# Optimization experiments

Measured on AMD Instinct MI355X. Metric: run time of the kernel, lower is better.

Reference implementation:

```python
import jax, jax.numpy as jnp
import numpy as np

EPS_D = 1e-8   # clamp_min on knn distances
EPS_BN = 1e-5  # BatchNorm eps
K = 3


def _cdist(a, b):
    # a: (B,M,3), b: (B,N,3) -> (B,M,N) euclidean distances
    a2 = jnp.sum(a * a, axis=-1)[:, :, None]
    b2 = jnp.sum(b * b, axis=-1)[:, None, :]
    ab = jnp.einsum('bmd,bnd->bmn', a, b)
    return jnp.sqrt(jnp.maximum(a2 + b2 - 2.0 * ab, 0.0))


def _bn_relu(x, gamma, beta):
    # x: (B,C,N); BatchNorm1d training-mode math (biased batch stats) + ReLU
    mean = jnp.mean(x, axis=(0, 2), keepdims=True)
    var = jnp.mean((x - mean) ** 2, axis=(0, 2), keepdims=True)
    xn = (x - mean) * jax.lax.rsqrt(var + EPS_BN)
    return jax.nn.relu(xn * gamma[None, :, None] + beta[None, :, None])


def setup_inputs() -> dict:
    key = jax.random.key(0)
    ks = jax.random.split(key, 6)
    B, N1, N2, C1, C2 = 8, 8192, 2048, 128, 256
    xyz1 = jax.random.normal(ks[0], (B, N1, 3), dtype=jnp.float32)
    xyz2 = jax.random.normal(ks[1], (B, N2, 3), dtype=jnp.float32)
    feats1 = jax.random.normal(ks[2], (B, C1, N1), dtype=jnp.float32)
    feats2 = jax.random.normal(ks[3], (B, C2, N2), dtype=jnp.float32)
    in_ch = C2 + C1  # 384
    W1 = jax.random.normal(ks[4], (256, in_ch), dtype=jnp.float32) * 0.05
    b1 = jnp.zeros((256,), jnp.float32)
    g1 = jnp.ones((256,), jnp.float32)
    be1 = jnp.zeros((256,), jnp.float32)
    W2 = jax.random.normal(ks[5], (128, 256), dtype=jnp.float32) * 0.05
    b2 = jnp.zeros((128,), jnp.float32)
    g2 = jnp.ones((128,), jnp.float32)
    be2 = jnp.zeros((128,), jnp.float32)
    return {"xyz1": xyz1, "xyz2": xyz2, "feats1": feats1, "feats2": feats2,
            "W1": W1, "b1": b1, "g1": g1, "be1": be1,
            "W2": W2, "b2": b2, "g2": g2, "be2": be2}


def reference(xyz1, xyz2, feats1, feats2, W1, b1, g1, be1, W2, b2, g2, be2):
    # --- KNN interpolation ---
    d = _cdist(xyz1, xyz2)                       # (B,N1,N2)
    _, idx = jax.lax.top_k(-d, K)                # smallest-K indices (B,N1,K)
    knn_d = jnp.take_along_axis(d, idx, axis=2)  # (B,N1,K)
    w = 1.0 / jnp.maximum(knn_d, EPS_D)
    w = w / jnp.sum(w, axis=-1, keepdims=True)
    f2p = jnp.swapaxes(feats2, 1, 2)             # (B,N2,C2)
    neigh = jax.vmap(lambda f, i: f[i])(f2p, idx)  # (B,N1,K,C2)
    out = jnp.einsum('bmk,bmkc->bmc', w, neigh)  # (B,N1,C2)
    out = jnp.swapaxes(out, 1, 2)                # (B,C2,N1)
    out = jnp.concatenate([out, feats1], axis=1) # (B,C2+C1,N1)
    # --- Conv1d(1)-BN-ReLU MLP ---
    h = jnp.einsum('oc,bcn->bon', W1, out) + b1[None, :, None]
    h = _bn_relu(h, g1, be1)
    h = jnp.einsum('oc,bcn->bon', W2, h) + b2[None, :, None]
    h = _bn_relu(h, g2, be2)
    return h
```

## Files before the change

kernel.cpp:

```cpp
#include <hip/hip_runtime.h>

typedef __attribute__((ext_vector_type(8))) short short8;
typedef __attribute__((ext_vector_type(4))) float f32x4;

#define GLDS(gp, lp) __builtin_amdgcn_global_load_lds( \
    (const __attribute__((address_space(1))) void*)(gp), \
    (__attribute__((address_space(3))) void*)(lp), 16, 0, 0)

__device__ __forceinline__ unsigned short f2bf(float f){
    unsigned u = __float_as_uint(f);
    unsigned r = (u + 0x7fffu + ((u >> 16) & 1u)) >> 16;
    return (unsigned short)r;
}
__device__ __forceinline__ float bf2f(unsigned short s){
    return __uint_as_float(((unsigned)s) << 16);
}

__global__ __launch_bounds__(256) void cast_w_kernel(const float* __restrict__ W1, const float* __restrict__ W2,
                                                     unsigned short* __restrict__ W1c, unsigned short* __restrict__ W2c){
    int i = blockIdx.x * 256 + threadIdx.x;
    if (i < 98304) W1c[i] = f2bf(W1[i]);
    if (i < 32768) W2c[i] = f2bf(W2[i]);
}

__global__ void zero_stats_kernel(float* __restrict__ s){
    int i = blockIdx.x * 256 + threadIdx.x;
    if (i < 768) s[i] = 0.f;
}

__global__ __launch_bounds__(256) void knn_kernel(const float* __restrict__ xyz1, const float* __restrict__ xyz2,
                                                  int* __restrict__ oi, float* __restrict__ ow){
    __shared__ float sx[2048], sy[2048], sz[2048];
    __shared__ float sd[64][25];
    __shared__ int   si[64][25];
    int blk = blockIdx.x;
    int b  = blk >> 7;
    int n0 = (blk & 127) << 6;
    const float* p2 = xyz2 + (size_t)b * 2048 * 3;
    for (int j = threadIdx.x; j < 2048; j += 256){
        sx[j] = p2[j*3+0]; sy[j] = p2[j*3+1]; sz[j] = p2[j*3+2];
    }
    __syncthreads();
    int pp = threadIdx.x & 31, sub = threadIdx.x >> 5;
    int pA = n0 + pp, pB = pA + 32;
    const float* qa = xyz1 + ((size_t)b * 8192 + pA) * 3;
    float ax = qa[0], ay = qa[1], az = qa[2];
    float bx = qa[96], by = qa[97], bz = qa[98];
    float A0 = 1e30f, A1 = 1e30f, A2 = 1e30f; int Ai0 = 0, Ai1 = 0, Ai2 = 0;
    float B0 = 1e30f, B1 = 1e30f, B2 = 1e30f; int Bi0 = 0, Bi1 = 0, Bi2 = 0;
    int jb = sub << 8;
#pragma unroll 2
    for (int i = 0; i < 256; i += 4){
        f32x4 cx = *(const f32x4*)&sx[jb + i];
        f32x4 cy = *(const f32x4*)&sy[jb + i];
        f32x4 cz = *(const f32x4*)&sz[jb + i];
#pragma unroll
        for (int u = 0; u < 4; ++u){
            int j = jb + i + u;
            float dxA = ax - cx[u], dyA = ay - cy[u], dzA = az - cz[u];
            float dA = fmaf(dxA, dxA, fmaf(dyA, dyA, dzA * dzA));
            float dxB = bx - cx[u], dyB = by - cy[u], dzB = bz - cz[u];
            float dB = fmaf(dxB, dxB, fmaf(dyB, dyB, dzB * dzB));
            if (dA < A2){
                if (dA < A1){
                    A2 = A1; Ai2 = Ai1;
                    if (dA < A0){ A1 = A0; Ai1 = Ai0; A0 = dA; Ai0 = j; }
                    else        { A1 = dA; Ai1 = j; }
                } else { A2 = dA; Ai2 = j; }
            }
            if (dB < B2){
                if (dB < B1){
                    B2 = B1; Bi2 = Bi1;
                    if (dB < B0){ B1 = B0; Bi1 = Bi0; B0 = dB; Bi0 = j; }
                    else        { B1 = dB; Bi1 = j; }
                } else { B2 = dB; Bi2 = j; }
            }
        }
    }
    int c = sub * 3;
    sd[pp][c] = A0; sd[pp][c+1] = A1; sd[pp][c+2] = A2;
    si[pp][c] = Ai0; si[pp][c+1] = Ai1; si[pp][c+2] = Ai2;
    sd[pp+32][c] = B0; sd[pp+32][c+1] = B1; sd[pp+32][c+2] = B2;
    si[pp+32][c] = Bi0; si[pp+32][c+1] = Bi1; si[pp+32][c+2] = Bi2;
    __syncthreads();
    if (threadIdx.x < 64){
        int lp = threadIdx.x;
        float d0 = 1e30f, d1 = 1e30f, d2 = 1e30f;
        int i0 = 0, i1 = 0, i2 = 0;
#pragma unroll
        for (int k = 0; k < 24; ++k){
            float d = sd[lp][k]; int j = si[lp][k];
            if (d < d2){
                if (d < d1){
                    d2 = d1; i2 = i1;
                    if (d < d0){ d1 = d0; i1 = i0; d0 = d; i0 = j; }
                    else        { d1 = d;  i1 = j; }
                } else { d2 = d; i2 = j; }
            }
        }
        float w0 = 1.f / fmaxf(sqrtf(d0), 1e-8f);
        float w1 = 1.f / fmaxf(sqrtf(d1), 1e-8f);
        float w2 = 1.f / fmaxf(sqrtf(d2), 1e-8f);
        float inv = 1.f / (w0 + w1 + w2);
        int n = n0 + lp;
        size_t pbase = ((size_t)b * 8192 + n) * 3;
        ow[pbase + 0] = w0 * inv; ow[pbase + 1] = w1 * inv; ow[pbase + 2] = w2 * inv;
        oi[pbase + 0] = i0;       oi[pbase + 1] = i1;       oi[pbase + 2] = i2;
    }
}

__global__ __launch_bounds__(256) void transpose_f2_kernel(const float* __restrict__ f2, unsigned short* __restrict__ f2t){
    __shared__ float tile[32][33];
    int b = blockIdx.z, c0 = blockIdx.y * 32, n0 = blockIdx.x * 32;
    int tx = threadIdx.x, ty = threadIdx.y;
    for (int i = 0; i < 32; i += 8)
        tile[ty + i][tx] = f2[((size_t)b * 256 + c0 + ty + i) * 2048 + n0 + tx];
    __syncthreads();
    for (int i = 0; i < 32; i += 8)
        f2t[((size_t)b * 2048 + n0 + ty + i) * 256 + c0 + tx] = f2bf(tile[tx][ty + i]);
}

__global__ __launch_bounds__(128) void interp_kernel(const int* __restrict__ ki, const float* __restrict__ kw,
                                                     const unsigned short* __restrict__ f2t, unsigned short* __restrict__ X){
    int p = blockIdx.x;
    int b = p >> 13;
    const int*   ip = ki + (size_t)p * 3;
    const float* wp = kw + (size_t)p * 3;
    int i0 = ip[0], i1 = ip[1], i2 = ip[2];
    float w0 = wp[0], w1 = wp[1], w2 = wp[2];
    int t = threadIdx.x;
    const unsigned* f0 = (const unsigned*)(f2t + ((size_t)b * 2048 + i0) * 256);
    const unsigned* f1 = (const unsigned*)(f2t + ((size_t)b * 2048 + i1) * 256);
    const unsigned* f2 = (const unsigned*)(f2t + ((size_t)b * 2048 + i2) * 256);
    unsigned a = f0[t], c = f1[t], d = f2[t];
    float r0 = w0 * bf2f((unsigned short)(a & 0xffff)) + w1 * bf2f((unsigned short)(c & 0xffff)) + w2 * bf2f((unsigned short)(d & 0xffff));
    float r1 = w0 * bf2f((unsigned short)(a >> 16))   + w1 * bf2f((unsigned short)(c >> 16))   + w2 * bf2f((unsigned short)(d >> 16));
    ((unsigned*)(X + (size_t)p * 384))[t] = (unsigned)f2bf(r0) | ((unsigned)f2bf(r1) << 16);
}

__global__ __launch_bounds__(256) void transpose_f1_kernel(const float* __restrict__ f1, unsigned short* __restrict__ X){
    __shared__ float tile[32][33];
    int b = blockIdx.z, c0 = blockIdx.y * 32, n0 = blockIdx.x * 32;
    int tx = threadIdx.x, ty = threadIdx.y;
    for (int i = 0; i < 32; i += 8)
        tile[ty + i][tx] = f1[((size_t)b * 128 + c0 + ty + i) * 8192 + n0 + tx];
    __syncthreads();
    for (int i = 0; i < 32; i += 8)
        X[((size_t)b * 8192 + n0 + ty + i) * 384 + 256 + c0 + tx] = f2bf(tile[tx][ty + i]);
}

template<int KT, bool OBF>
__global__ __launch_bounds__(256) void gemm_bt(const unsigned short* __restrict__ A, const unsigned short* __restrict__ Bt,
                                               const float* __restrict__ bias, void* __restrict__ Cout,
                                               float* __restrict__ gsum, float* __restrict__ gsq, int Ncols){
    __shared__ unsigned short As[128 * 32];
    __shared__ unsigned short Bs[128 * 32];
    __shared__ float sLs[128], sLq[128];
    int tid = threadIdx.x;
    if (tid < 128){ sLs[tid] = 0.f; sLq[tid] = 0.f; }
    int m0 = blockIdx.x * 128;
    int n0 = blockIdx.y * 128;
    int lane = tid & 63, wid = tid >> 6;
    int m_w = (wid >> 1) * 64, n_w = (wid & 1) * 64;
    f32x4 acc[4][4] = {};

    int srow = tid >> 2, schunk = tid & 3;
    const char* Ab = (const char*)A + ((size_t)(m0 + srow) * KT + schunk * 8) * 2;
    const char* Bb = (const char*)Bt + ((size_t)(n0 + srow) * KT + schunk * 8) * 2;
    char* Asl = (char*)As + tid * 16;
    char* Bsl = (char*)Bs + tid * 16;
    const size_t rstep = (size_t)64 * KT * 2;

    int lr = lane & 15, lq = lane >> 4;
    for (int kt = 0; kt < KT / 32; ++kt){
        size_t koff = (size_t)kt * 64;
        GLDS(Ab + koff, Asl);
        GLDS(Ab + koff + rstep, Asl + 4096);
        GLDS(Bb + koff, Bsl);
        GLDS(Bb + koff + rstep, Bsl + 4096);
        __syncthreads();
        short8 af[4], bfr[4];
#pragma unroll
        for (int mf = 0; mf < 4; ++mf)
            af[mf] = *(const short8*)(As + (m_w + mf * 16 + lr) * 32 + lq * 8);
#pragma unroll
        for (int nf = 0; nf < 4; ++nf)
            bfr[nf] = *(const short8*)(Bs + (n_w + nf * 16 + lr) * 32 + lq * 8);
#pragma unroll
        for (int mf = 0; mf < 4; ++mf)
#pragma unroll
            for (int nf = 0; nf < 4; ++nf)
                acc[mf][nf] = __builtin_amdgcn_mfma_f32_16x16x32_bf16(af[mf], bfr[nf], acc[mf][nf], 0, 0, 0);
        __syncthreads();
    }

#pragma unroll
    for (int nf = 0; nf < 4; ++nf){
        int cl = n_w + nf * 16 + lr;
        int gc = n0 + cl;
        float bv = bias[gc];
        float ps = 0.f, pq = 0.f;
#pragma unroll
        for (int mf = 0; mf < 4; ++mf){
            int grow = m0 + m_w + mf * 16 + lq * 4;
#pragma unroll
            for (int r = 0; r < 4; ++r){
                float v = acc[mf][nf][r] + bv;
                size_t off = (size_t)(grow + r) * Ncols + gc;
                if (OBF) ((unsigned short*)Cout)[off] = f2bf(v);
                else     ((float*)Cout)[off] = v;
                ps += v; pq += v * v;
            }
        }
        ps += __shfl_xor(ps, 16); ps += __shfl_xor(ps, 32);
        pq += __shfl_xor(pq, 16); pq += __shfl_xor(pq, 32);
        if (lq == 0){ atomicAdd(&sLs[cl], ps); atomicAdd(&sLq[cl], pq); }
    }
    __syncthreads();
    if (tid < 128){
        atomicAdd(&gsum[n0 + tid], sLs[tid]);
        atomicAdd(&gsq[n0 + tid],  sLq[tid]);
    }
}

__global__ __launch_bounds__(256) void bn_relu_bf16(unsigned short* __restrict__ h, const float* __restrict__ gsum,
                                                    const float* __restrict__ gsq, const float* __restrict__ gamma,
                                                    const float* __restrict__ beta){
    const float inv = 1.0f / 65536.0f;
    size_t total2 = (size_t)65536 * 128;
    unsigned* hp = (unsigned*)h;
    for (size_t i = (size_t)blockIdx.x * blockDim.x + threadIdx.x; i < total2; i += (size_t)gridDim.x * blockDim.x){
        int c0 = (int)((i * 2) & 255);
        unsigned v = hp[i];
        float x0 = bf2f((unsigned short)(v & 0xffff));
        float x1 = bf2f((unsigned short)(v >> 16));
        float m0 = gsum[c0] * inv,     m1 = gsum[c0 + 1] * inv;
        float va0 = gsq[c0] * inv - m0 * m0, va1 = gsq[c0 + 1] * inv - m1 * m1;
        float rs0 = rsqrtf(va0 + 1e-5f), rs1 = rsqrtf(va1 + 1e-5f);
        float y0 = fmaxf((x0 - m0) * rs0 * gamma[c0] + beta[c0], 0.f);
        float y1 = fmaxf((x1 - m1) * rs1 * gamma[c0 + 1] + beta[c0 + 1], 0.f);
        hp[i] = (unsigned)f2bf(y0) | ((unsigned)f2bf(y1) << 16);
    }
}

__global__ __launch_bounds__(256) void bn2_transpose_kernel(const float* __restrict__ h2, const float* __restrict__ gsum,
                                                            const float* __restrict__ gsq, const float* __restrict__ g2,
                                                            const float* __restrict__ be2, float* __restrict__ out){
    __shared__ float tile[32][33];
    const float inv = 1.0f / 65536.0f;
    int b = blockIdx.z, o0 = blockIdx.y * 32, n0 = blockIdx.x * 32;
    int tx = threadIdx.x, ty = threadIdx.y;
    for (int i = 0; i < 32; i += 8)
        tile[ty + i][tx] = h2[((size_t)b * 8192 + n0 + ty + i) * 128 + o0 + tx];
    __syncthreads();
    for (int i = 0; i < 32; i += 8){
        int ch = o0 + ty + i;
        float m = gsum[ch] * inv;
        float va = gsq[ch] * inv - m * m;
        float rs = rsqrtf(va + 1e-5f);
        float sc = g2[ch] * rs, sh = be2[ch] - m * sc;
        float v = fmaxf(tile[tx][ty + i] * sc + sh, 0.f);
        out[((size_t)b * 128 + ch) * 8192 + n0 + tx] = v;
    }
}

extern "C" void kernel_launch(void* const* d_in, const int* in_sizes, int n_in,
                              void* d_out, int out_size, void* d_ws, size_t ws_size,
                              hipStream_t stream){
    const float* xyz1   = (const float*)d_in[0];
    const float* xyz2   = (const float*)d_in[1];
    const float* feats1 = (const float*)d_in[2];
    const float* feats2 = (const float*)d_in[3];
    const float* W1  = (const float*)d_in[4];
    const float* b1  = (const float*)d_in[5];
    const float* g1  = (const float*)d_in[6];
    const float* be1 = (const float*)d_in[7];
    const float* W2  = (const float*)d_in[8];
    const float* b2  = (const float*)d_in[9];
    const float* g2  = (const float*)d_in[10];
    const float* be2 = (const float*)d_in[11];
    float* out = (float*)d_out;

    char* p = (char*)d_ws;
    auto take = [&](size_t bytes) -> char* {
        char* r = p; p += (bytes + 255) & ~(size_t)255; return r;
    };
    unsigned short* W1c = (unsigned short*)take((size_t)98304 * 2);
    unsigned short* W2c = (unsigned short*)take((size_t)32768 * 2);
    int*   ki    = (int*)take((size_t)65536 * 3 * 4);
    float* kw    = (float*)take((size_t)65536 * 3 * 4);
    float* stats = (float*)take(768 * 4);
    unsigned short* f2t = (unsigned short*)take((size_t)8 * 2048 * 256 * 2);
    unsigned short* X   = (unsigned short*)take((size_t)65536 * 384 * 2);
    unsigned short* h1  = (unsigned short*)take((size_t)65536 * 256 * 2);
    float* h2 = (float*)X;

    float* s1 = stats, *q1 = stats + 256, *s2 = stats + 512, *q2 = stats + 640;

    zero_stats_kernel<<<dim3(3), 256, 0, stream>>>(stats);
    cast_w_kernel<<<dim3(384), 256, 0, stream>>>(W1, W2, W1c, W2c);
    knn_kernel<<<dim3(1024), 256, 0, stream>>>(xyz1, xyz2, ki, kw);
    transpose_f2_kernel<<<dim3(64, 8, 8), dim3(32, 8), 0, stream>>>(feats2, f2t);
    interp_kernel<<<dim3(65536), 128, 0, stream>>>(ki, kw, f2t, X);
    transpose_f1_kernel<<<dim3(256, 4, 8), dim3(32, 8), 0, stream>>>(feats1, X);
    gemm_bt<384, true><<<dim3(512, 2), 256, 0, stream>>>(X, W1c, b1, h1, s1, q1, 256);
    bn_relu_bf16<<<dim3(2048), 256, 0, stream>>>(h1, s1, q1, g1, be1);
    gemm_bt<256, false><<<dim3(512, 1), 256, 0, stream>>>(h1, W2c, b2, h2, s2, q2, 128);
    bn2_transpose_kernel<<<dim3(256, 4, 8), dim3(32, 8), 0, stream>>>(h2, s2, q2, g2, be2, out);
}
```

Baseline: 300.7 us.

## Fuse KNN interpolation into GEMM1 prologue and BN1-ReLU into GEMM2 A-load

Drops the standalone interpolation kernel and the 384-wide concatenated X buffer. The first GEMM now gathers the three neighbour rows, blends them by weight and loads feats1 directly into shared memory while W1 streams in through global_load_lds. It also covers all 256 output channels per block so the gather is not repeated. A small kernel folds the BN1 statistics into scale and shift, which GEMM2 applies with ReLU as it loads h1, removing the in-place bn_relu pass and two kernel launches. The cost is register-heavy accumulators (4x8 tiles), A-tile loads that are no longer asynchronous, and scattered gathers in the GEMM's critical path.

Result: faster. 258.7 us (-14.0%).

```diff
diff --git a/kernel.cpp b/kernel.cpp
--- a/kernel.cpp
+++ b/kernel.cpp
@@ -16,16 +16,13 @@
     return __uint_as_float(((unsigned)s) << 16);
 }
 
-__global__ __launch_bounds__(256) void cast_w_kernel(const float* __restrict__ W1, const float* __restrict__ W2,
-                                                     unsigned short* __restrict__ W1c, unsigned short* __restrict__ W2c){
+__global__ __launch_bounds__(256) void init_kernel(const float* __restrict__ W1, const float* __restrict__ W2,
+                                                   unsigned short* __restrict__ W1c, unsigned short* __restrict__ W2c,
+                                                   float* __restrict__ stats){
     int i = blockIdx.x * 256 + threadIdx.x;
     if (i < 98304) W1c[i] = f2bf(W1[i]);
     if (i < 32768) W2c[i] = f2bf(W2[i]);
-}
-
-__global__ void zero_stats_kernel(float* __restrict__ s){
-    int i = blockIdx.x * 256 + threadIdx.x;
-    if (i < 768) s[i] = 0.f;
+    if (i < 768) stats[i] = 0.f;
 }
 
 __global__ __launch_bounds__(256) void knn_kernel(const float* __restrict__ xyz1, const float* __restrict__ xyz2,
@@ -42,7 +39,7 @@
     }
     __syncthreads();
     int pp = threadIdx.x & 31, sub = threadIdx.x >> 5;
-    int pA = n0 + pp, pB = pA + 32;
+    int pA = n0 + pp;
     const float* qa = xyz1 + ((size_t)b * 8192 + pA) * 3;
     float ax = qa[0], ay = qa[1], az = qa[2];
     float bx = qa[96], by = qa[97], bz = qa[98];
@@ -120,25 +117,7 @@
         f2t[((size_t)b * 2048 + n0 + ty + i) * 256 + c0 + tx] = f2bf(tile[tx][ty + i]);
 }
 
-__global__ __launch_bounds__(128) void interp_kernel(const int* __restrict__ ki, const float* __restrict__ kw,
-                                                     const unsigned short* __restrict__ f2t, unsigned short* __restrict__ X){
-    int p = blockIdx.x;
-    int b = p >> 13;
-    const int*   ip = ki + (size_t)p * 3;
-    const float* wp = kw + (size_t)p * 3;
-    int i0 = ip[0], i1 = ip[1], i2 = ip[2];
-    float w0 = wp[0], w1 = wp[1], w2 = wp[2];
-    int t = threadIdx.x;
-    const unsigned* f0 = (const unsigned*)(f2t + ((size_t)b * 2048 + i0) * 256);
-    const unsigned* f1 = (const unsigned*)(f2t + ((size_t)b * 2048 + i1) * 256);
-    const unsigned* f2 = (const unsigned*)(f2t + ((size_t)b * 2048 + i2) * 256);
-    unsigned a = f0[t], c = f1[t], d = f2[t];
-    float r0 = w0 * bf2f((unsigned short)(a & 0xffff)) + w1 * bf2f((unsigned short)(c & 0xffff)) + w2 * bf2f((unsigned short)(d & 0xffff));
-    float r1 = w0 * bf2f((unsigned short)(a >> 16))   + w1 * bf2f((unsigned short)(c >> 16))   + w2 * bf2f((unsigned short)(d >> 16));
-    ((unsigned*)(X + (size_t)p * 384))[t] = (unsigned)f2bf(r0) | ((unsigned)f2bf(r1) << 16);
-}
-
-__global__ __launch_bounds__(256) void transpose_f1_kernel(const float* __restrict__ f1, unsigned short* __restrict__ X){
+__global__ __launch_bounds__(256) void transpose_f1_kernel(const float* __restrict__ f1, unsigned short* __restrict__ f1t){
     __shared__ float tile[32][33];
     int b = blockIdx.z, c0 = blockIdx.y * 32, n0 = blockIdx.x * 32;
     int tx = threadIdx.x, ty = threadIdx.y;
@@ -146,43 +125,206 @@
         tile[ty + i][tx] = f1[((size_t)b * 128 + c0 + ty + i) * 8192 + n0 + tx];
     __syncthreads();
     for (int i = 0; i < 32; i += 8)
-        X[((size_t)b * 8192 + n0 + ty + i) * 384 + 256 + c0 + tx] = f2bf(tile[tx][ty + i]);
-}
-
-template<int KT, bool OBF>
-__global__ __launch_bounds__(256) void gemm_bt(const unsigned short* __restrict__ A, const unsigned short* __restrict__ Bt,
-                                               const float* __restrict__ bias, void* __restrict__ Cout,
-                                               float* __restrict__ gsum, float* __restrict__ gsq, int Ncols){
-    __shared__ unsigned short As[128 * 32];
+        f1t[((size_t)b * 8192 + n0 + ty + i) * 128 + c0 + tx] = f2bf(tile[tx][ty + i]);
+}
+
+__global__ __launch_bounds__(256, 2) void gemm1_fused(const unsigned short* __restrict__ f2t,
+                                                      const unsigned short* __restrict__ f1t,
+                                                      const int* __restrict__ ki, const float* __restrict__ kw,
+                                                      const unsigned short* __restrict__ W1c,
+                                                      const float* __restrict__ bias,
+                                                      unsigned short* __restrict__ h1,
+                                                      float* __restrict__ gsum, float* __restrict__ gsq){
+    __shared__ unsigned short As[128 * 40];
+    __shared__ unsigned short Bs[256 * 32];
+    __shared__ int   sIdx[384];
+    __shared__ float sW[384];
+    __shared__ float sLs[256], sLq[256];
+    int tid = threadIdx.x;
+    int m0 = blockIdx.x << 7;
+    int b  = blockIdx.x >> 6;
+    for (int i = tid; i < 384; i += 256){ sIdx[i] = ki[(size_t)m0 * 3 + i]; sW[i] = kw[(size_t)m0 * 3 + i]; }
+    sLs[tid] = 0.f; sLq[tid] = 0.f;
+    __syncthreads();
+
+    int pt = tid >> 1, hh = tid & 1;
+    int i0 = sIdx[pt*3], i1 = sIdx[pt*3+1], i2 = sIdx[pt*3+2];
+    float w0 = sW[pt*3], w1 = sW[pt*3+1], w2 = sW[pt*3+2];
+    const unsigned short* r0 = f2t + (((size_t)b * 2048 + i0) << 8);
+    const unsigned short* r1 = f2t + (((size_t)b * 2048 + i1) << 8);
+    const unsigned short* r2 = f2t + (((size_t)b * 2048 + i2) << 8);
+    const unsigned short* f1row = f1t + ((size_t)(m0 + pt) << 7);
+    unsigned short* awp = As + pt * 40 + hh * 16;
+
+    int srow = tid >> 2, schunk = tid & 3;
+    const char* Bb = (const char*)W1c + ((size_t)srow * 384 + schunk * 8) * 2;
+    char* Bsl = (char*)Bs + tid * 16;
+
+    int lane = tid & 63, wid = tid >> 6;
+    int m_w = (wid >> 1) * 64, n_w = (wid & 1) * 128;
+    int lr = lane & 15, lq = lane >> 4;
+    f32x4 acc[4][8] = {};
+
+    for (int kt = 0; kt < 12; ++kt){
+        size_t ko = (size_t)kt * 64;
+        GLDS(Bb + ko,                 Bsl);
+        GLDS(Bb + ko + (size_t)49152, Bsl + 4096);
+        GLDS(Bb + ko + (size_t)98304, Bsl + 8192);
+        GLDS(Bb + ko + (size_t)147456, Bsl + 12288);
+        if (kt < 8){
+            int cb = kt * 32 + hh * 16;
+            uint4 a0 = *(const uint4*)(r0 + cb);
+            uint4 a1 = *(const uint4*)(r0 + cb + 8);
+            uint4 c0 = *(const uint4*)(r1 + cb);
+            uint4 c1 = *(const uint4*)(r1 + cb + 8);
+            uint4 d0 = *(const uint4*)(r2 + cb);
+            uint4 d1 = *(const uint4*)(r2 + cb + 8);
+            uint4 o0, o1;
+            const unsigned* ap = (const unsigned*)&a0; const unsigned* cp = (const unsigned*)&c0;
+            const unsigned* dp = (const unsigned*)&d0; unsigned* op = (unsigned*)&o0;
+#pragma unroll
+            for (int u = 0; u < 4; ++u){
+                float lo = w0 * bf2f((unsigned short)(ap[u] & 0xffff))
+                         + w1 * bf2f((unsigned short)(cp[u] & 0xffff))
+                         + w2 * bf2f((unsigned short)(dp[u] & 0xffff));
+                float hi = w0 * bf2f((unsigned short)(ap[u] >> 16))
+                         + w1 * bf2f((unsigned short)(cp[u] >> 16))
+                         + w2 * bf2f((unsigned short)(dp[u] >> 16));
+                op[u] = (unsigned)f2bf(lo) | ((unsigned)f2bf(hi) << 16);
+            }
+            ap = (const unsigned*)&a1; cp = (const unsigned*)&c1;
+            dp = (const unsigned*)&d1; op = (unsigned*)&o1;
+#pragma unroll
+            for (int u = 0; u < 4; ++u){
+                float lo = w0 * bf2f((unsigned short)(ap[u] & 0xffff))
+                         + w1 * bf2f((unsigned short)(cp[u] & 0xffff))
+                         + w2 * bf2f((unsigned short)(dp[u] & 0xffff));
+                float hi = w0 * bf2f((unsigned short)(ap[u] >> 16))
+                         + w1 * bf2f((unsigned short)(cp[u] >> 16))
+                         + w2 * bf2f((unsigned short)(dp[u] >> 16));
+                op[u] = (unsigned)f2bf(lo) | ((unsigned)f2bf(hi) << 16);
+            }
+            *(uint4*)awp = o0;
+            *(uint4*)(awp + 8) = o1;
+        } else {
+            int cb = (kt - 8) * 32 + hh * 16;
+            uint4 v0 = *(const uint4*)(f1row + cb);
+            uint4 v1 = *(const uint4*)(f1row + cb + 8);
+            *(uint4*)awp = v0;
+            *(uint4*)(awp + 8) = v1;
+        }
+        __syncthreads();
+        short8 af[4], bfr[8];
+#pragma unroll
+        for (int mf = 0; mf < 4; ++mf)
+            af[mf] = *(const short8*)(As + (m_w + mf * 16 + lr) * 40 + lq * 8);
+#pragma unroll
+        for (int nf = 0; nf < 8; ++nf)
+            bfr[nf] = *(const short8*)(Bs + (n_w + nf * 16 + lr) * 32 + lq * 8);
+#pragma unroll
+        for (int mf = 0; mf < 4; ++mf)
+#pragma unroll
+            for (int nf = 0; nf < 8; ++nf)
+                acc[mf][nf] = __builtin_amdgcn_mfma_f32_16x16x32_bf16(af[mf], bfr[nf], acc[mf][nf], 0, 0, 0);
+        __syncthreads();
+    }
+
+#pragma unroll
+    for (int nf = 0; nf < 8; ++nf){
+        int gc = n_w + nf * 16 + lr;
+        float bv = bias[gc];
+        float ps = 0.f, pq = 0.f;
+#pragma unroll
+        for (int mf = 0; mf < 4; ++mf){
+            int grow = m0 + m_w + mf * 16 + lq * 4;
+#pragma unroll
+            for (int r = 0; r < 4; ++r){
+                float v = acc[mf][nf][r] + bv;
+                h1[(size_t)(grow + r) * 256 + gc] = f2bf(v);
+                ps += v; pq += v * v;
+            }
+        }
+        ps += __shfl_xor(ps, 16); ps += __shfl_xor(ps, 32);
+        pq += __shfl_xor(pq, 16); pq += __shfl_xor(pq, 32);
+        if (lq == 0){ atomicAdd(&sLs[gc], ps); atomicAdd(&sLq[gc], pq); }
+    }
+    __syncthreads();
+    atomicAdd(&gsum[tid], sLs[tid]);
+    atomicAdd(&gsq[tid],  sLq[tid]);
+}
+
+__global__ void bnprep_kernel(const float* __restrict__ s1, const float* __restrict__ q1,
+                              const float* __restrict__ g1, const float* __restrict__ be1,
+                              float* __restrict__ sc, float* __restrict__ sh){
+    int c = threadIdx.x;
+    const float inv = 1.0f / 65536.0f;
+    float m = s1[c] * inv;
+    float v = q1[c] * inv - m * m;
+    float rs = rsqrtf(v + 1e-5f);
+    float s = g1[c] * rs;
+    sc[c] = s; sh[c] = be1[c] - m * s;
+}
+
+__global__ __launch_bounds__(256, 2) void gemm2_fused(const unsigned short* __restrict__ h1,
+                                                      const unsigned short* __restrict__ W2c,
+                                                      const float* __restrict__ bias,
+                                                      const float* __restrict__ sc1, const float* __restrict__ sh1,
+                                                      float* __restrict__ h2,
+                                                      float* __restrict__ gsum, float* __restrict__ gsq){
+    __shared__ unsigned short As[128 * 40];
     __shared__ unsigned short Bs[128 * 32];
+    __shared__ float ssc[256], ssh[256];
     __shared__ float sLs[128], sLq[128];
     int tid = threadIdx.x;
+    int m0 = blockIdx.x << 7;
+    ssc[tid] = sc1[tid]; ssh[tid] = sh1[tid];
     if (tid < 128){ sLs[tid] = 0.f; sLq[tid] = 0.f; }
-    int m0 = blockIdx.x * 128;
-    int n0 = blockIdx.y * 128;
+    __syncthreads();
+
+    int pt = tid >> 1, hh = tid & 1;
+    const unsigned short* hrow = h1 + ((size_t)(m0 + pt) << 8);
+    unsigned short* awp = As + pt * 40 + hh * 16;
+
+    int srow = tid >> 2, schunk = tid & 3;
+    const char* Bb = (const char*)W2c + ((size_t)srow * 256 + schunk * 8) * 2;
+    char* Bsl = (char*)Bs + tid * 16;
+
     int lane = tid & 63, wid = tid >> 6;
     int m_w = (wid >> 1) * 64, n_w = (wid & 1) * 64;
+    int lr = lane & 15, lq = lane >> 4;
     f32x4 acc[4][4] = {};
 
-    int srow = tid >> 2, schunk = tid & 3;
-    const char* Ab = (const char*)A + ((size_t)(m0 + srow) * KT + schunk * 8) * 2;
-    const char* Bb = (const char*)Bt + ((size_t)(n0 + srow) * KT + schunk * 8) * 2;
-    char* Asl = (char*)As + tid * 16;
-    char* Bsl = (char*)Bs + tid * 16;
-    const size_t rstep = (size_t)64 * KT * 2;
-
-    int lr = lane & 15, lq = lane >> 4;
-    for (int kt = 0; kt < KT / 32; ++kt){
-        size_t koff = (size_t)kt * 64;
-        GLDS(Ab + koff, Asl);
-        GLDS(Ab + koff + rstep, Asl + 4096);
-        GLDS(Bb + koff, Bsl);
-        GLDS(Bb + koff + rstep, Bsl + 4096);
+    for (int kt = 0; kt < 8; ++kt){
+        size_t ko = (size_t)kt * 64;
+        GLDS(Bb + ko,                Bsl);
+        GLDS(Bb + ko + (size_t)32768, Bsl + 4096);
+        int cb = kt * 32 + hh * 16;
+        uint4 v0 = *(const uint4*)(hrow + cb);
+        uint4 v1 = *(const uint4*)(hrow + cb + 8);
+        uint4 o0, o1;
+        const unsigned* vp = (const unsigned*)&v0; unsigned* op = (unsigned*)&o0;
+#pragma unroll
+        for (int u = 0; u < 4; ++u){
+            int cc = cb + 2 * u;
+            float lo = fmaxf(bf2f((unsigned short)(vp[u] & 0xffff)) * ssc[cc]     + ssh[cc],     0.f);
+            float hi = fmaxf(bf2f((unsigned short)(vp[u] >> 16))    * ssc[cc + 1] + ssh[cc + 1], 0.f);
+            op[u] = (unsigned)f2bf(lo) | ((unsigned)f2bf(hi) << 16);
+        }
+        vp = (const unsigned*)&v1; op = (unsigned*)&o1;
+#pragma unroll
+        for (int u = 0; u < 4; ++u){
+            int cc = cb + 8 + 2 * u;
+            float lo = fmaxf(bf2f((unsigned short)(vp[u] & 0xffff)) * ssc[cc]     + ssh[cc],     0.f);
+            float hi = fmaxf(bf2f((unsigned short)(vp[u] >> 16))    * ssc[cc + 1] + ssh[cc + 1], 0.f);
+            op[u] = (unsigned)f2bf(lo) | ((unsigned)f2bf(hi) << 16);
+        }
+        *(uint4*)awp = o0;
+        *(uint4*)(awp + 8) = o1;
         __syncthreads();
         short8 af[4], bfr[4];
 #pragma unroll
         for (int mf = 0; mf < 4; ++mf)
-            af[mf] = *(const short8*)(As + (m_w + mf * 16 + lr) * 32 + lq * 8);
+            af[mf] = *(const short8*)(As + (m_w + mf * 16 + lr) * 40 + lq * 8);
 #pragma unroll
         for (int nf = 0; nf < 4; ++nf)
             bfr[nf] = *(const short8*)(Bs + (n_w + nf * 16 + lr) * 32 + lq * 8);
@@ -196,8 +338,7 @@
 
 #pragma unroll
     for (int nf = 0; nf < 4; ++nf){
-        int cl = n_w + nf * 16 + lr;
-        int gc = n0 + cl;
+        int gc = n_w + nf * 16 + lr;
         float bv = bias[gc];
         float ps = 0.f, pq = 0.f;
 #pragma unroll
@@ -206,40 +347,18 @@
 #pragma unroll
             for (int r = 0; r < 4; ++r){
                 float v = acc[mf][nf][r] + bv;
-                size_t off = (size_t)(grow + r) * Ncols + gc;
-                if (OBF) ((unsigned short*)Cout)[off] = f2bf(v);
-                else     ((float*)Cout)[off] = v;
+                h2[(size_t)(grow + r) * 128 + gc] = v;
                 ps += v; pq += v * v;
             }
         }
         ps += __shfl_xor(ps, 16); ps += __shfl_xor(ps, 32);
         pq += __shfl_xor(pq, 16); pq += __shfl_xor(pq, 32);
-        if (lq == 0){ atomicAdd(&sLs[cl], ps); atomicAdd(&sLq[cl], pq); }
+        if (lq == 0){ atomicAdd(&sLs[gc], ps); atomicAdd(&sLq[gc], pq); }
     }
     __syncthreads();
     if (tid < 128){
-        atomicAdd(&gsum[n0 + tid], sLs[tid]);
-        atomicAdd(&gsq[n0 + tid],  sLq[tid]);
-    }
-}
-
-__global__ __launch_bounds__(256) void bn_relu_bf16(unsigned short* __restrict__ h, const float* __restrict__ gsum,
-                                                    const float* __restrict__ gsq, const float* __restrict__ gamma,
-                                                    const float* __restrict__ beta){
-    const float inv = 1.0f / 65536.0f;
-    size_t total2 = (size_t)65536 * 128;
-    unsigned* hp = (unsigned*)h;
-    for (size_t i = (size_t)blockIdx.x * blockDim.x + threadIdx.x; i < total2; i += (size_t)gridDim.x * blockDim.x){
-        int c0 = (int)((i * 2) & 255);
-        unsigned v = hp[i];
-        float x0 = bf2f((unsigned short)(v & 0xffff));
-        float x1 = bf2f((unsigned short)(v >> 16));
-        float m0 = gsum[c0] * inv,     m1 = gsum[c0 + 1] * inv;
-        float va0 = gsq[c0] * inv - m0 * m0, va1 = gsq[c0 + 1] * inv - m1 * m1;
-        float rs0 = rsqrtf(va0 + 1e-5f), rs1 = rsqrtf(va1 + 1e-5f);
-        float y0 = fmaxf((x0 - m0) * rs0 * gamma[c0] + beta[c0], 0.f);
-        float y1 = fmaxf((x1 - m1) * rs1 * gamma[c0 + 1] + beta[c0 + 1], 0.f);
-        hp[i] = (unsigned)f2bf(y0) | ((unsigned)f2bf(y1) << 16);
+        atomicAdd(&gsum[tid], sLs[tid]);
+        atomicAdd(&gsq[tid],  sLq[tid]);
     }
 }
 
@@ -290,21 +409,21 @@
     int*   ki    = (int*)take((size_t)65536 * 3 * 4);
     float* kw    = (float*)take((size_t)65536 * 3 * 4);
     float* stats = (float*)take(768 * 4);
+    float* scsh  = (float*)take(512 * 4);
     unsigned short* f2t = (unsigned short*)take((size_t)8 * 2048 * 256 * 2);
-    unsigned short* X   = (unsigned short*)take((size_t)65536 * 384 * 2);
+    unsigned short* f1t = (unsigned short*)take((size_t)65536 * 128 * 2);
     unsigned short* h1  = (unsigned short*)take((size_t)65536 * 256 * 2);
-    float* h2 = (float*)X;
+    float* h2 = (float*)take((size_t)65536 * 128 * 4);
 
     float* s1 = stats, *q1 = stats + 256, *s2 = stats + 512, *q2 = stats + 640;
-
-    zero_stats_kernel<<<dim3(3), 256, 0, stream>>>(stats);
-    cast_w_kernel<<<dim3(384), 256, 0, stream>>>(W1, W2, W1c, W2c);
+    float* sc1 = scsh, *sh1 = scsh + 256;
+
+    init_kernel<<<dim3(384), 256, 0, stream>>>(W1, W2, W1c, W2c, stats);
     knn_kernel<<<dim3(1024), 256, 0, stream>>>(xyz1, xyz2, ki, kw);
     transpose_f2_kernel<<<dim3(64, 8, 8), dim3(32, 8), 0, stream>>>(feats2, f2t);
-    interp_kernel<<<dim3(65536), 128, 0, stream>>>(ki, kw, f2t, X);
-    transpose_f1_kernel<<<dim3(256, 4, 8), dim3(32, 8), 0, stream>>>(feats1, X);
-    gemm_bt<384, true><<<dim3(512, 2), 256, 0, stream>>>(X, W1c, b1, h1, s1, q1, 256);
-    bn_relu_bf16<<<dim3(2048), 256, 0, stream>>>(h1, s1, q1, g1, be1);
-    gemm_bt<256, false><<<dim3(512, 1), 256, 0, stream>>>(h1, W2c, b2, h2, s2, q2, 128);
+    transpose_f1_kernel<<<dim3(256, 4, 8), dim3(32, 8), 0, stream>>>(feats1, f1t);
+    gemm1_fused<<<dim3(512), 256, 0, stream>>>(f2t, f1t, ki, kw, W1c, b1, h1, s1, q1);
+    bnprep_kernel<<<dim3(1), 256, 0, stream>>>(s1, q1, g1, be1, sc1, sh1);
+    gemm2_fused<<<dim3(512), 256, 0, stream>>>(h1, W2c, b2, sc1, sh1, h2, s2, q2);
     bn2_transpose_kernel<<<dim3(256, 4, 8), dim3(32, 8), 0, stream>>>(h2, s2, q2, g2, be2, out);
 }
```
